# Optimization experiments

Hardware: AMD Instinct MI355X
Metric: run time of the kernel (lower is better)

Reference implementation:

```python
import jax, jax.numpy as jnp
import numpy as np

N_NODES = 50000
N_EDGES = 800000
N_GRAPHS = 32
IN_DIM = 3
HID = 128
EDGE_DIM = 3
OUT_DIM = 40
N_LAYERS = 3
EPS = 1e-5
SLOPE = 0.2  # GATv2 leaky_relu negative_slope


def setup_inputs() -> dict:
    key = jax.random.key(0)
    ks = jax.random.split(key, 24)
    s = lambda fan: 1.0 / np.sqrt(fan)
    inp = {
        "x": jax.random.normal(ks[0], (N_NODES, IN_DIM), jnp.float32),
        "edge_attr": jax.random.normal(ks[1], (N_EDGES, EDGE_DIM), jnp.float32),
        "edge_index": jax.random.randint(ks[2], (2, N_EDGES), 0, N_NODES),
        "batch": jnp.sort(jax.random.randint(ks[3], (N_NODES,), 0, N_GRAPHS)),
        # layer 0 (in_dim -> hid, separate lin_l / lin_r)
        "W0l": jax.random.normal(ks[4], (IN_DIM, HID), jnp.float32) * s(IN_DIM),
        "W0r": jax.random.normal(ks[5], (IN_DIM, HID), jnp.float32) * s(IN_DIM),
        "We0": jax.random.normal(ks[6], (EDGE_DIM, HID), jnp.float32) * s(EDGE_DIM),
        "a0": jax.random.normal(ks[7], (HID,), jnp.float32) * s(HID),
        "b0": jnp.zeros((HID,), jnp.float32),
        "bn0_g": jnp.ones((HID,), jnp.float32),
        "bn0_b": jnp.zeros((HID,), jnp.float32),
        # layers 1..n-1 (hid -> hid, share_weights=True -> single W per layer)
        "W": jax.random.normal(ks[8], (N_LAYERS - 1, HID, HID), jnp.float32) * s(HID),
        "We": jax.random.normal(ks[9], (N_LAYERS - 1, EDGE_DIM, HID), jnp.float32) * s(EDGE_DIM),
        "a": jax.random.normal(ks[10], (N_LAYERS - 1, HID), jnp.float32) * s(HID),
        "b": jnp.zeros((N_LAYERS - 1, HID), jnp.float32),
        "bn_g": jnp.ones((N_LAYERS - 1, HID), jnp.float32),
        "bn_b": jnp.zeros((N_LAYERS - 1, HID), jnp.float32),
        # FC classifier head (Linear-ReLU-Linear)
        "fc1_W": jax.random.normal(ks[11], (HID, HID), jnp.float32) * s(HID),
        "fc1_b": jnp.zeros((HID,), jnp.float32),
        "fc2_W": jax.random.normal(ks[12], (HID, OUT_DIM), jnp.float32) * s(HID),
        "fc2_b": jnp.zeros((OUT_DIM,), jnp.float32),
    }
    return inp


def _self_loop_attr(edge_attr, dst):
    # PyG add_self_loops(fill_value='mean'): per-node mean of incoming edge_attr
    cnt = jax.ops.segment_sum(jnp.ones((edge_attr.shape[0],), edge_attr.dtype), dst, num_segments=N_NODES)
    tot = jax.ops.segment_sum(edge_attr, dst, num_segments=N_NODES)
    return tot / jnp.maximum(cnt, 1.0)[:, None]


def _gatv2(x, src, dst, eattr, Wl, Wr, We, att, bias):
    xl = x @ Wl                                   # [N,H] source transform
    xr = x @ Wr                                   # [N,H] target transform
    e = eattr @ We                                # [E2,H]
    m = jax.nn.leaky_relu(xl[src] + xr[dst] + e, SLOPE)
    logit = m @ att                               # [E2]
    lmax = jax.ops.segment_max(logit, dst, num_segments=N_NODES)
    ex = jnp.exp(logit - lmax[dst])
    den = jax.ops.segment_sum(ex, dst, num_segments=N_NODES)
    alpha = ex / den[dst]
    out = jax.ops.segment_sum(alpha[:, None] * xl[src], dst, num_segments=N_NODES)
    return out + bias


def _bn(h, g, b):
    mu = h.mean(0)
    var = jnp.mean((h - mu) ** 2, 0)
    return g * (h - mu) * jax.lax.rsqrt(var + EPS) + b


def reference(x, edge_attr, edge_index, batch, W0l, W0r, We0, a0, b0, bn0_g, bn0_b,
              W, We, a, b, bn_g, bn_b, fc1_W, fc1_b, fc2_W, fc2_b):
    src, dst = edge_index[0], edge_index[1]
    loop = jnp.arange(N_NODES)
    loop_attr = _self_loop_attr(edge_attr, dst)
    src2 = jnp.concatenate([src, loop])
    dst2 = jnp.concatenate([dst, loop])
    eattr2 = jnp.concatenate([edge_attr, loop_attr], axis=0)

    h = _gatv2(x, src2, dst2, eattr2, W0l, W0r, We0, a0, b0)
    h = _bn(jax.nn.relu(h), bn0_g, bn0_b)
    for i in range(N_LAYERS - 1):  # share_weights=True: Wl == Wr == W[i]
        h = _gatv2(h, src2, dst2, eattr2, W[i], W[i], We[i], a[i], b[i])
        h = _bn(jax.nn.relu(h), bn_g[i], bn_b[i])

    pooled = jax.ops.segment_max(h, batch, num_segments=N_GRAPHS)  # [G,H]
    z = jax.nn.relu(pooled @ fc1_W + fc1_b)
    return z @ fc2_W + fc2_b  # [G, OUT_DIM]
```

## Files before the change

### kernel.cpp

```cpp
#include <hip/hip_runtime.h>

#define NN 50000
#define NE 800000
#define NG 32
#define HID 128
#define BNEPS 1e-5f
#define NETOT (NE + NN)

typedef float f32x2 __attribute__((ext_vector_type(2)));
typedef float f32x4 __attribute__((ext_vector_type(4)));
typedef short bf16x8 __attribute__((ext_vector_type(8)));

__device__ __forceinline__ unsigned fenc(float f) {
  unsigned u = __float_as_uint(f);
  return (u & 0x80000000u) ? ~u : (u | 0x80000000u);
}

__device__ __forceinline__ unsigned bfr(float f) {
  unsigned u = __float_as_uint(f);
  return (u + 0x7fffu + ((u >> 16) & 1u)) >> 16;
}
__device__ __forceinline__ unsigned pack2(float a, float b) {
  return bfr(a) | (bfr(b) << 16);
}
__device__ __forceinline__ float bf_lo(unsigned u) { return __uint_as_float(u << 16); }
__device__ __forceinline__ float bf_hi(unsigned u) { return __uint_as_float(u & 0xffff0000u); }

#define DPPADD(x, ctrl, rmask)                                                   \
  (x) += __int_as_float(__builtin_amdgcn_update_dpp(0, __float_as_int(x),        \
                                                    (ctrl), (rmask), 0xf, true))


__global__ __launch_bounds__(256) void k_hist(const int* __restrict__ ei,
                                              int* __restrict__ deg,
                                              int* __restrict__ pos) {
  int e = blockIdx.x * 256 + threadIdx.x;
  if (e >= NE) return;
  pos[e] = atomicAdd(&deg[ei[NE + e]], 1);
}

__global__ __launch_bounds__(1024) void k_scanA(const int* __restrict__ deg,
                                                int* __restrict__ rowp,
                                                int* __restrict__ bsum) {
  __shared__ int wsum[16];
  int t = threadIdx.x, lane = t & 63, w = t >> 6;
  int i = blockIdx.x * 1024 + t;
  int v = (i < NN) ? (deg[i] + 1) : 0;
  int s = v;
#pragma unroll
  for (int off = 1; off < 64; off <<= 1) {
    int y = __shfl_up(s, off, 64);
    if (lane >= off) s += y;
  }
  if (lane == 63) wsum[w] = s;
  __syncthreads();
  if (t < 16) {
    int xv = wsum[t];
#pragma unroll
    for (int off = 1; off < 16; off <<= 1) {
      int y = __shfl_up(xv, off, 64);
      if (t >= off) xv += y;
    }
    wsum[t] = xv;
  }
  __syncthreads();
  int wexcl = (w == 0) ? 0 : wsum[w - 1];
  int incl = wexcl + s;
  if (i < NN) rowp[i] = incl - v;
  if (t == 1023) bsum[blockIdx.x] = incl;
}

__global__ __launch_bounds__(64) void k_scanB(int* __restrict__ bsum,
                                              int* __restrict__ rowp,
                                              uint2* __restrict__ edat) {
  int t = threadIdx.x;
  int v = (t < 49) ? bsum[t] : 0;
  int s = v;
#pragma unroll
  for (int off = 1; off < 64; off <<= 1) {
    int y = __shfl_up(s, off, 64);
    if (t >= off) s += y;
  }
  bsum[t] = s - v;
  if (t == 48) rowp[NN] = s;
  for (int j = t; j < 256; j += 64) {
    uint2 z; z.x = 0u; z.y = 0u;
    edat[NETOT + j] = z;
  }
}

__global__ __launch_bounds__(1024) void k_scanC(int* __restrict__ rowp,
                                                const int* __restrict__ bsum) {
  int i = blockIdx.x * 1024 + threadIdx.x;
  if (i < NN) rowp[i] += bsum[blockIdx.x];
}

__global__ __launch_bounds__(256) void k_scatter(const int* __restrict__ ei,
    const float* __restrict__ eattr, const int* __restrict__ rowp,
    const int* __restrict__ pos, uint2* __restrict__ edat) {
  int e = blockIdx.x * 256 + threadIdx.x;
  if (e >= NE) return;
  int d = ei[NE + e];
  int p = rowp[d] + pos[e];
  uint2 v;
  v.x = (unsigned)ei[e] | (bfr(eattr[e * 3 + 0]) << 16);
  v.y = bfr(eattr[e * 3 + 1]) | (bfr(eattr[e * 3 + 2]) << 16);
  edat[p] = v;
}

__global__ __launch_bounds__(256) void k_selfmean(const int* __restrict__ rowp,
                                                  uint2* __restrict__ edat) {
  int n = blockIdx.x * 256 + threadIdx.x;
  if (n >= NN) return;
  int beg = rowp[n], endm1 = rowp[n + 1] - 1;
  float s0 = 0.f, s1 = 0.f, s2 = 0.f;
  for (int i = beg; i < endm1; ++i) {
    uint2 v = edat[i];
    s0 += bf_hi(v.x); s1 += bf_lo(v.y); s2 += bf_hi(v.y);
  }
  int cnt = endm1 - beg;
  float inv = cnt > 0 ? 1.f / (float)cnt : 0.f;
  uint2 o;
  o.x = (unsigned)n | (bfr(s0 * inv) << 16);
  o.y = bfr(s1 * inv) | (bfr(s2 * inv) << 16);
  edat[endm1] = o;
}


__global__ __launch_bounds__(256) void k_xform0(const float* __restrict__ x,
    const float* __restrict__ W0l, const float* __restrict__ W0r,
    unsigned* __restrict__ A, unsigned* __restrict__ B) {
  int t = blockIdx.x * 256 + threadIdx.x;
  int n = t >> 5;
  int c = (t & 31) * 4;
  if (n >= NN) return;
  float x0 = x[n * 3 + 0], x1 = x[n * 3 + 1], x2 = x[n * 3 + 2];
  float4 a0 = *(const float4*)&W0l[c];
  float4 a1 = *(const float4*)&W0l[HID + c];
  float4 a2 = *(const float4*)&W0l[2 * HID + c];
  float oax = x0 * a0.x + x1 * a1.x + x2 * a2.x;
  float oay = x0 * a0.y + x1 * a1.y + x2 * a2.y;
  float oaz = x0 * a0.z + x1 * a1.z + x2 * a2.z;
  float oaw = x0 * a0.w + x1 * a1.w + x2 * a2.w;
  uint2 pa;
  pa.x = pack2(oax, oay);
  pa.y = pack2(oaz, oaw);
  *(uint2*)&A[n * 64 + (c >> 1)] = pa;
  float4 b0 = *(const float4*)&W0r[c];
  float4 b1 = *(const float4*)&W0r[HID + c];
  float4 b2 = *(const float4*)&W0r[2 * HID + c];
  float obx = x0 * b0.x + x1 * b1.x + x2 * b2.x;
  float oby = x0 * b0.y + x1 * b1.y + x2 * b2.y;
  float obz = x0 * b0.z + x1 * b1.z + x2 * b2.z;
  float obw = x0 * b0.w + x1 * b1.w + x2 * b2.w;
  uint2 pb;
  pb.x = pack2(obx, oby);
  pb.y = pack2(obz, obw);
  *(uint2*)&B[n * 64 + (c >> 1)] = pb;
}


__global__ __launch_bounds__(256) void k_wprep(const float* __restrict__ W,
    const float* __restrict__ cs, const float* __restrict__ g,
    const float* __restrict__ b, unsigned* __restrict__ Wt,
    float* __restrict__ bias2) {
  __shared__ float scS[HID], shS[HID];
  int t = threadIdx.x;
  if (t < HID) {
    float mu = cs[t] * (1.f / NN);
    float var = fmaxf(cs[HID + t] * (1.f / NN) - mu * mu, 0.f);
    float sc = g[t] * rsqrtf(var + BNEPS);
    scS[t] = sc;
    shS[t] = b[t] - mu * sc;
  }
  __syncthreads();
  for (int i = t; i < HID * 64; i += 256) {
    int n = i >> 6, kp = (i & 63) * 2;
    Wt[i] = pack2(scS[kp] * W[kp * HID + n], scS[kp + 1] * W[(kp + 1) * HID + n]);
  }
  if (t < HID) {
    float acc = 0.f;
    for (int k = 0; k < HID; ++k) acc += shS[k] * W[k * HID + t];
    bias2[t] = acc;
  }
}


__global__ __launch_bounds__(256) void k_gemm(const unsigned* __restrict__ Hb,
    const unsigned* __restrict__ Wt, const float* __restrict__ bias2,
    unsigned* __restrict__ A) {
  __shared__ unsigned WsL[HID * 68];
  int t = threadIdx.x;
  for (int i = t; i < HID * 64; i += 256)
    WsL[(i >> 6) * 68 + (i & 63)] = Wt[i];
  __syncthreads();
  int l = t & 63;
  int w = t >> 6;
  int r0 = blockIdx.x * 64 + w * 16;
  int l15 = l & 15;
  int arow = min(r0 + l15, NN - 1);
  int kg = (l >> 4) * 4;
  float bl[8];
#pragma unroll
  for (int nt = 0; nt < 8; ++nt) bl[nt] = bias2[nt * 16 + l15];
  f32x4 acc[8] = {};
#pragma unroll
  for (int ks = 0; ks < 4; ++ks) {
    uint4 au = *(const uint4*)&Hb[arow * 64 + ks * 16 + kg];
    au.x &= ~(((au.x >> 15) & 0x10001u) * 0xFFFFu);
    au.y &= ~(((au.y >> 15) & 0x10001u) * 0xFFFFu);
    au.z &= ~(((au.z >> 15) & 0x10001u) * 0xFFFFu);
    au.w &= ~(((au.w >> 15) & 0x10001u) * 0xFFFFu);
    bf16x8 af = *(bf16x8*)&au;
#pragma unroll
    for (int nt = 0; nt < 8; ++nt) {
      uint4 bu = *(const uint4*)&WsL[(nt * 16 + l15) * 68 + ks * 16 + kg];
      bf16x8 bf = *(bf16x8*)&bu;
      acc[nt] = __builtin_amdgcn_mfma_f32_16x16x32_bf16(af, bf, acc[nt], 0, 0, 0);
    }
  }
#pragma unroll
  for (int nt = 0; nt < 8; ++nt) {
#pragma unroll
    for (int reg = 0; reg < 4; ++reg) {
      float v = acc[nt][reg] + bl[nt];
      float nb = __shfl_down(v, 1, 64);
      int rm = r0 + (l >> 4) * 4 + reg;
      if (((l & 1) == 0) && rm < NN)
        A[rm * 64 + nt * 8 + (l15 >> 1)] = pack2(v, nb);
    }
  }
}


__global__ __launch_bounds__(256) void k_edge(const unsigned* __restrict__ XL,
    const unsigned* __restrict__ XR, const uint2* __restrict__ edat,
    const int* __restrict__ rowp, const float* __restrict__ We,
    const float* __restrict__ att, const float* __restrict__ bias,
    unsigned* __restrict__ Hb) {
  __shared__ float WeS[3 * HID];
  int t = threadIdx.x;
  for (int i = t; i < 3 * HID; i += 256) WeS[i] = We[i];
  __syncthreads();
  int lane = t & 63;
  int l4 = lane & 15;
  int n = blockIdx.x * 16 + (t >> 6) * 4 + (lane >> 4);
  int c0 = l4 * 8;
  uint4 urx = *(const uint4*)&XR[n * 64 + l4 * 4];
  f32x2 xr0 = {bf_lo(urx.x), bf_hi(urx.x)};
  f32x2 xr1 = {bf_lo(urx.y), bf_hi(urx.y)};
  f32x2 xr2 = {bf_lo(urx.z), bf_hi(urx.z)};
  f32x2 xr3 = {bf_lo(urx.w), bf_hi(urx.w)};
  f32x2 at0 = *(const f32x2*)&att[c0];
  f32x2 at1 = *(const f32x2*)&att[c0 + 2];
  f32x2 at2 = *(const f32x2*)&att[c0 + 4];
  f32x2 at3 = *(const f32x2*)&att[c0 + 6];
  at0 *= 1.44269504f; at1 *= 1.44269504f; at2 *= 1.44269504f; at3 *= 1.44269504f;
  f32x2 w00 = *(const f32x2*)&WeS[c0],         w01 = *(const f32x2*)&WeS[c0 + 2];
  f32x2 w02 = *(const f32x2*)&WeS[c0 + 4],     w03 = *(const f32x2*)&WeS[c0 + 6];
  f32x2 w10 = *(const f32x2*)&WeS[HID + c0],   w11 = *(const f32x2*)&WeS[HID + c0 + 2];
  f32x2 w12 = *(const f32x2*)&WeS[HID + c0+4], w13 = *(const f32x2*)&WeS[HID + c0 + 6];
  f32x2 w20 = *(const f32x2*)&WeS[2*HID + c0],   w21 = *(const f32x2*)&WeS[2*HID + c0 + 2];
  f32x2 w22 = *(const f32x2*)&WeS[2*HID + c0+4], w23 = *(const f32x2*)&WeS[2*HID + c0 + 6];
  int beg = rowp[n], end = rowp[n + 1];
  int rem = end - beg;
  int tc = rem;
  tc = max(tc, __shfl_xor(tc, 16, 64));
  tc = max(tc, __shfl_xor(tc, 32, 64));
  int trips = (__builtin_amdgcn_readfirstlane(tc) + 3) & ~3;
  const unsigned* XLg = XL + l4 * 4;

  uint2 e0 = edat[beg], e1 = edat[beg + 1], e2 = edat[beg + 2], e3 = edat[beg + 3];
  uint4 x0 = *(const uint4*)&XLg[(e0.x & 0xffffu) * 64];
  uint4 x1 = *(const uint4*)&XLg[(e1.x & 0xffffu) * 64];
  uint4 x2, x3;
  f32x2 a0 = {0.f, 0.f}, a1 = {0.f, 0.f}, a2 = {0.f, 0.f}, a3 = {0.f, 0.f};
  float s = 0.f;

#define BODY(ED, XU, J)                                                           \
  {                                                                               \
    f32x2 xs0 = {bf_lo(XU.x), bf_hi(XU.x)};                                       \
    f32x2 xs1 = {bf_lo(XU.y), bf_hi(XU.y)};                                       \
    f32x2 xs2 = {bf_lo(XU.z), bf_hi(XU.z)};                                       \
    f32x2 xs3 = {bf_lo(XU.w), bf_hi(XU.w)};                                       \
    float ea0 = bf_hi(ED.x), ea1 = bf_lo(ED.y), ea2 = bf_hi(ED.y);                \
    f32x2 u0 = xs0 + xr0, u1 = xs1 + xr1, u2 = xs2 + xr2, u3 = xs3 + xr3;         \
    u0 = ea0 * w00 + u0; u1 = ea0 * w01 + u1; u2 = ea0 * w02 + u2; u3 = ea0 * w03 + u3; \
    u0 = ea1 * w10 + u0; u1 = ea1 * w11 + u1; u2 = ea1 * w12 + u2; u3 = ea1 * w13 + u3; \
    u0 = ea2 * w20 + u0; u1 = ea2 * w21 + u1; u2 = ea2 * w22 + u2; u3 = ea2 * w23 + u3; \
    f32x2 v0 = __builtin_elementwise_max(u0, 0.2f * u0);                          \
    f32x2 v1 = __builtin_elementwise_max(u1, 0.2f * u1);                          \
    f32x2 v2 = __builtin_elementwise_max(u2, 0.2f * u2);                          \
    f32x2 v3 = __builtin_elementwise_max(u3, 0.2f * u3);                          \
    f32x2 pl = v0 * at0;                                                          \
    pl = v1 * at1 + pl;                                                           \
    pl = v2 * at2 + pl;                                                           \
    pl = v3 * at3 + pl;                                                           \
    float part = pl.x + pl.y;                                                     \
    DPPADD(part, 0x121, 0xf);                                      \
    DPPADD(part, 0x122, 0xf);                                      \
    DPPADD(part, 0x124, 0xf);                                      \
    DPPADD(part, 0x128, 0xf);        \
    float p = __builtin_amdgcn_exp2f(part);                                       \
    p = (i + (J) < rem) ? p : 0.f;                                                \
    s += p;                                                                       \
    a0 = p * xs0 + a0; a1 = p * xs1 + a1;                                         \
    a2 = p * xs2 + a2; a3 = p * xs3 + a3;                                         \
  }

  for (int i = 0; i < trips; i += 4) {
    x2 = *(const uint4*)&XLg[(e2.x & 0xffffu) * 64];
    BODY(e0, x0, 0);
    e0 = edat[beg + i + 4];
    x3 = *(const uint4*)&XLg[(e3.x & 0xffffu) * 64];
    BODY(e1, x1, 1);
    e1 = edat[beg + i + 5];
    x0 = *(const uint4*)&XLg[(e0.x & 0xffffu) * 64];
    BODY(e2, x2, 2);
    e2 = edat[beg + i + 6];
    x1 = *(const uint4*)&XLg[(e1.x & 0xffffu) * 64];
    BODY(e3, x3, 3);
    e3 = edat[beg + i + 7];
  }
#undef BODY

  float inv = 1.f / s;
  f32x2 b0 = *(const f32x2*)&bias[c0];
  f32x2 b1 = *(const f32x2*)&bias[c0 + 2];
  f32x2 b2 = *(const f32x2*)&bias[c0 + 4];
  f32x2 b3 = *(const f32x2*)&bias[c0 + 6];
  f32x2 o0 = a0 * inv + b0;
  f32x2 o1 = a1 * inv + b1;
  f32x2 o2 = a2 * inv + b2;
  f32x2 o3 = a3 * inv + b3;
  uint4 o;
  o.x = pack2(o0.x, o0.y);
  o.y = pack2(o1.x, o1.y);
  o.z = pack2(o2.x, o2.y);
  o.w = pack2(o3.x, o3.y);
  *(uint4*)&Hb[n * 64 + l4 * 4] = o;
}


__global__ __launch_bounds__(256) void k_bnstats(const unsigned* __restrict__ Hb,
                                                 float* __restrict__ cs) {
  __shared__ float red[8][256];
  int t = threadIdx.x;
  int ui = (t & 31) * 2;
  int c0 = ui * 2;
  int grp = t >> 5;
  int chunk = (NN + gridDim.x - 1) / gridDim.x;
  int n0 = blockIdx.x * chunk, n1 = min(n0 + chunk, NN);
  float s10 = 0.f, s11 = 0.f, s12 = 0.f, s13 = 0.f;
  float s20 = 0.f, s21 = 0.f, s22 = 0.f, s23 = 0.f;
  for (int n = n0 + grp; n < n1; n += 8) {
    uint2 h = *(const uint2*)&Hb[n * 64 + ui];
    float v0 = fmaxf(bf_lo(h.x), 0.f), v1 = fmaxf(bf_hi(h.x), 0.f);
    float v2 = fmaxf(bf_lo(h.y), 0.f), v3 = fmaxf(bf_hi(h.y), 0.f);
    s10 += v0; s11 += v1; s12 += v2; s13 += v3;
    s20 += v0 * v0; s21 += v1 * v1; s22 += v2 * v2; s23 += v3 * v3;
  }
  red[grp][c0 + 0] = s10; red[grp][c0 + 1] = s11;
  red[grp][c0 + 2] = s12; red[grp][c0 + 3] = s13;
  red[grp][128 + c0 + 0] = s20; red[grp][128 + c0 + 1] = s21;
  red[grp][128 + c0 + 2] = s22; red[grp][128 + c0 + 3] = s23;
  __syncthreads();
  float sum = 0.f;
#pragma unroll
  for (int g2 = 0; g2 < 8; ++g2) sum += red[g2][t];
  atomicAdd(&cs[t], sum);
}


__global__ __launch_bounds__(256) void k_pool(const unsigned* __restrict__ Hb,
    const int* __restrict__ batch, const float* __restrict__ cs,
    const float* __restrict__ g, const float* __restrict__ b,
    unsigned* __restrict__ pooled) {
  int t = threadIdx.x;
  int ui = (t & 31) * 2;
  int c0 = ui * 2;
  int grp = t >> 5;
  float scv0, scv1, scv2, scv3, shv0, shv1, shv2, shv3;
  {
    float mu, var;
    mu = cs[c0 + 0] * (1.f / NN); var = fmaxf(cs[HID + c0 + 0] * (1.f / NN) - mu * mu, 0.f);
    scv0 = g[c0 + 0] * rsqrtf(var + BNEPS); shv0 = b[c0 + 0] - mu * scv0;
    mu = cs[c0 + 1] * (1.f / NN); var = fmaxf(cs[HID + c0 + 1] * (1.f / NN) - mu * mu, 0.f);
    scv1 = g[c0 + 1] * rsqrtf(var + BNEPS); shv1 = b[c0 + 1] - mu * scv1;
    mu = cs[c0 + 2] * (1.f / NN); var = fmaxf(cs[HID + c0 + 2] * (1.f / NN) - mu * mu, 0.f);
    scv2 = g[c0 + 2] * rsqrtf(var + BNEPS); shv2 = b[c0 + 2] - mu * scv2;
    mu = cs[c0 + 3] * (1.f / NN); var = fmaxf(cs[HID + c0 + 3] * (1.f / NN) - mu * mu, 0.f);
    scv3 = g[c0 + 3] * rsqrtf(var + BNEPS); shv3 = b[c0 + 3] - mu * scv3;
  }
  int chunk = (NN + gridDim.x - 1) / gridDim.x;
  int n0 = blockIdx.x * chunk, n1 = min(n0 + chunk, NN);
  int curg = -1;
  float m0 = -3.402823e38f, m1 = m0, m2 = m0, m3 = m0;
  for (int n = n0 + grp; n < n1; n += 8) {
    int gg = batch[n];
    if (gg != curg) {
      if (curg >= 0) {
        atomicMax(&pooled[curg * HID + c0 + 0], fenc(m0));
        atomicMax(&pooled[curg * HID + c0 + 1], fenc(m1));
        atomicMax(&pooled[curg * HID + c0 + 2], fenc(m2));
        atomicMax(&pooled[curg * HID + c0 + 3], fenc(m3));
      }
      curg = gg;
      m0 = m1 = m2 = m3 = -3.402823e38f;
    }
    uint2 h = *(const uint2*)&Hb[n * 64 + ui];
    m0 = fmaxf(m0, fmaxf(bf_lo(h.x), 0.f) * scv0 + shv0);
    m1 = fmaxf(m1, fmaxf(bf_hi(h.x), 0.f) * scv1 + shv1);
    m2 = fmaxf(m2, fmaxf(bf_lo(h.y), 0.f) * scv2 + shv2);
    m3 = fmaxf(m3, fmaxf(bf_hi(h.y), 0.f) * scv3 + shv3);
  }
  if (curg >= 0) {
    atomicMax(&pooled[curg * HID + c0 + 0], fenc(m0));
    atomicMax(&pooled[curg * HID + c0 + 1], fenc(m1));
    atomicMax(&pooled[curg * HID + c0 + 2], fenc(m2));
    atomicMax(&pooled[curg * HID + c0 + 3], fenc(m3));
  }
}


__global__ __launch_bounds__(128) void k_fc(const unsigned* __restrict__ pooled,
    const float* __restrict__ W1, const float* __restrict__ b1,
    const float* __restrict__ W2, const float* __restrict__ b2,
    float* __restrict__ out) {
  __shared__ float P[HID];
  __shared__ float Z[HID];
  int g = blockIdx.x, c = threadIdx.x;
  unsigned k = pooled[g * HID + c];
  P[c] = (k & 0x80000000u) ? __uint_as_float(k ^ 0x80000000u) : __uint_as_float(~k);
  __syncthreads();
  float acc = b1[c];
  for (int kk = 0; kk < HID; ++kk) acc += P[kk] * W1[kk * HID + c];
  Z[c] = fmaxf(acc, 0.f);
  __syncthreads();
  if (c < 40) {
    float a2 = b2[c];
    for (int kk = 0; kk < HID; ++kk) a2 += Z[kk] * W2[kk * 40 + c];
    out[g * 40 + c] = a2;
  }
}


extern "C" void kernel_launch(void* const* d_in, const int* in_sizes, int n_in,
                              void* d_out, int out_size, void* d_ws, size_t ws_size,
                              hipStream_t stream) {
  (void)in_sizes; (void)n_in; (void)out_size; (void)ws_size;
  const float* x     = (const float*)d_in[0];
  const float* eattr = (const float*)d_in[1];
  const int*   ei    = (const int*)d_in[2];
  const int*   batch = (const int*)d_in[3];
  const float* W0l   = (const float*)d_in[4];
  const float* W0r   = (const float*)d_in[5];
  const float* We0   = (const float*)d_in[6];
  const float* a0    = (const float*)d_in[7];
  const float* b0    = (const float*)d_in[8];
  const float* bn0g  = (const float*)d_in[9];
  const float* bn0b  = (const float*)d_in[10];
  const float* Wl    = (const float*)d_in[11];
  const float* Wel   = (const float*)d_in[12];
  const float* al    = (const float*)d_in[13];
  const float* bl    = (const float*)d_in[14];
  const float* bng   = (const float*)d_in[15];
  const float* bnb   = (const float*)d_in[16];
  const float* fc1W  = (const float*)d_in[17];
  const float* fc1b  = (const float*)d_in[18];
  const float* fc2W  = (const float*)d_in[19];
  const float* fc2b  = (const float*)d_in[20];
  float* out = (float*)d_out;

  char* ws = (char*)d_ws;
  unsigned* Hbf  = (unsigned*)(ws + 0);
  unsigned* Abf  = (unsigned*)(ws + 12800000);
  unsigned* X0bf = (unsigned*)(ws + 25600000);
  uint2*    edat = (uint2*)(ws + 38400000);
  int*      rowp = (int*)(ws + 45202048);
  int*      pos  = (int*)(ws + 45402112);
  char*     zb   = ws + 48602112;
  int*      deg  = (int*)(zb + 0);
  float*    cs   = (float*)(zb + 200000);
  unsigned* pooled = (unsigned*)(zb + 203072);
  int*      bsum = (int*)(zb + 219456);
  const size_t ZLEN = 219712;
  unsigned* wtb   = (unsigned*)(ws + 48821824);
  float*    bias2 = (float*)(ws + 48854592);

  hipMemsetAsync(zb, 0, ZLEN, stream);

  k_hist<<<(NE + 255) / 256, 256, 0, stream>>>(ei, deg, pos);
  k_scanA<<<49, 1024, 0, stream>>>(deg, rowp, bsum);
  k_scanB<<<1, 64, 0, stream>>>(bsum, rowp, edat);
  k_scanC<<<49, 1024, 0, stream>>>(rowp, bsum);
  k_scatter<<<(NE + 255) / 256, 256, 0, stream>>>(ei, eattr, rowp, pos, edat);
  k_selfmean<<<(NN + 255) / 256, 256, 0, stream>>>(rowp, edat);

  k_xform0<<<(NN * 32) / 256, 256, 0, stream>>>(x, W0l, W0r, Abf, X0bf);
  k_edge<<<(NN + 15) / 16, 256, 0, stream>>>(Abf, X0bf, edat, rowp, We0, a0, b0, Hbf);
  k_bnstats<<<512, 256, 0, stream>>>(Hbf, cs);

  k_wprep<<<1, 256, 0, stream>>>(Wl, cs, bn0g, bn0b, wtb, bias2);
  k_gemm<<<(NN + 63) / 64, 256, 0, stream>>>(Hbf, wtb, bias2, Abf);
  k_edge<<<(NN + 15) / 16, 256, 0, stream>>>(Abf, Abf, edat, rowp, Wel, al, bl, Hbf);
  k_bnstats<<<512, 256, 0, stream>>>(Hbf, cs + 256);

  k_wprep<<<1, 256, 0, stream>>>(Wl + 128 * 128, cs + 256, bng, bnb, wtb, bias2);
  k_gemm<<<(NN + 63) / 64, 256, 0, stream>>>(Hbf, wtb, bias2, Abf);
  k_edge<<<(NN + 15) / 16, 256, 0, stream>>>(Abf, Abf, edat, rowp, Wel + 384, al + 128, bl + 128, Hbf);
  k_bnstats<<<512, 256, 0, stream>>>(Hbf, cs + 512);

  k_pool<<<512, 256, 0, stream>>>(Hbf, batch, cs + 512, bng + 128, bnb + 128, pooled);
  k_fc<<<NG, 128, 0, stream>>>(pooled, fc1W, fc1b, fc2W, fc2b, out);
}
```

Before: 358.0 us.

## Sort destination nodes by in-degree to balance edge-kernel wavefronts

```diff
diff --git a/kernel.cpp b/kernel.cpp
--- a/kernel.cpp
+++ b/kernel.cpp
@@ -39,13 +39,60 @@
   pos[e] = atomicAdd(&deg[ei[NE + e]], 1);
 }
 
+
+__global__ __launch_bounds__(256) void k_dhist(const int* __restrict__ deg,
+                                               int* __restrict__ dhist) {
+  int n = blockIdx.x * 256 + threadIdx.x;
+  if (n >= NN) return;
+  atomicAdd(&dhist[min(deg[n], 1023)], 1);
+}
+
+__global__ __launch_bounds__(1024) void k_dscan(const int* __restrict__ dhist,
+                                                int* __restrict__ dbase) {
+  __shared__ int wsum[16];
+  int t = threadIdx.x, lane = t & 63, w = t >> 6;
+  int v = dhist[t];
+  int s = v;
+#pragma unroll
+  for (int off = 1; off < 64; off <<= 1) {
+    int y = __shfl_up(s, off, 64);
+    if (lane >= off) s += y;
+  }
+  if (lane == 63) wsum[w] = s;
+  __syncthreads();
+  if (t < 16) {
+    int xv = wsum[t];
+#pragma unroll
+    for (int off = 1; off < 16; off <<= 1) {
+      int y = __shfl_up(xv, off, 64);
+      if (t >= off) xv += y;
+    }
+    wsum[t] = xv;
+  }
+  __syncthreads();
+  int incl = s + ((w == 0) ? 0 : wsum[w - 1]);
+  dbase[t] = NN - incl;
+}
+
+__global__ __launch_bounds__(256) void k_dscatter(const int* __restrict__ deg,
+    const int* __restrict__ dbase, int* __restrict__ dfill,
+    int* __restrict__ ord, int* __restrict__ rank) {
+  int n = blockIdx.x * 256 + threadIdx.x;
+  if (n >= NN) return;
+  int d = min(deg[n], 1023);
+  int p = dbase[d] + atomicAdd(&dfill[d], 1);
+  ord[p] = n;
+  rank[n] = p;
+}
+
 __global__ __launch_bounds__(1024) void k_scanA(const int* __restrict__ deg,
+                                                const int* __restrict__ ord,
                                                 int* __restrict__ rowp,
                                                 int* __restrict__ bsum) {
   __shared__ int wsum[16];
   int t = threadIdx.x, lane = t & 63, w = t >> 6;
   int i = blockIdx.x * 1024 + t;
-  int v = (i < NN) ? (deg[i] + 1) : 0;
+  int v = (i < NN) ? (deg[ord[i]] + 1) : 0;
   int s = v;
 #pragma unroll
   for (int off = 1; off < 64; off <<= 1) {
@@ -97,11 +144,12 @@
 
 __global__ __launch_bounds__(256) void k_scatter(const int* __restrict__ ei,
     const float* __restrict__ eattr, const int* __restrict__ rowp,
-    const int* __restrict__ pos, uint2* __restrict__ edat) {
+    const int* __restrict__ pos, const int* __restrict__ rank,
+    uint2* __restrict__ edat) {
   int e = blockIdx.x * 256 + threadIdx.x;
   if (e >= NE) return;
   int d = ei[NE + e];
-  int p = rowp[d] + pos[e];
+  int p = rowp[rank[d]] + pos[e];
   uint2 v;
   v.x = (unsigned)ei[e] | (bfr(eattr[e * 3 + 0]) << 16);
   v.y = bfr(eattr[e * 3 + 1]) | (bfr(eattr[e * 3 + 2]) << 16);
@@ -109,6 +157,7 @@
 }
 
 __global__ __launch_bounds__(256) void k_selfmean(const int* __restrict__ rowp,
+                                                  const int* __restrict__ ord,
                                                   uint2* __restrict__ edat) {
   int n = blockIdx.x * 256 + threadIdx.x;
   if (n >= NN) return;
@@ -121,7 +170,7 @@
   int cnt = endm1 - beg;
   float inv = cnt > 0 ? 1.f / (float)cnt : 0.f;
   uint2 o;
-  o.x = (unsigned)n | (bfr(s0 * inv) << 16);
+  o.x = (unsigned)ord[n] | (bfr(s0 * inv) << 16);
   o.y = bfr(s1 * inv) | (bfr(s2 * inv) << 16);
   edat[endm1] = o;
 }
@@ -191,43 +240,47 @@
     unsigned* __restrict__ A) {
   __shared__ unsigned WsL[HID * 68];
   int t = threadIdx.x;
-  for (int i = t; i < HID * 64; i += 256)
-    WsL[(i >> 6) * 68 + (i & 63)] = Wt[i];
+  for (int i4 = t * 4; i4 < HID * 64; i4 += 1024) {
+    uint4 v = *(const uint4*)&Wt[i4];
+    *(uint4*)&WsL[(i4 >> 6) * 68 + (i4 & 63)] = v;
+  }
   __syncthreads();
   int l = t & 63;
   int w = t >> 6;
-  int r0 = blockIdx.x * 64 + w * 16;
   int l15 = l & 15;
-  int arow = min(r0 + l15, NN - 1);
   int kg = (l >> 4) * 4;
   float bl[8];
 #pragma unroll
   for (int nt = 0; nt < 8; ++nt) bl[nt] = bias2[nt * 16 + l15];
-  f32x4 acc[8] = {};
-#pragma unroll
-  for (int ks = 0; ks < 4; ++ks) {
-    uint4 au = *(const uint4*)&Hb[arow * 64 + ks * 16 + kg];
-    au.x &= ~(((au.x >> 15) & 0x10001u) * 0xFFFFu);
-    au.y &= ~(((au.y >> 15) & 0x10001u) * 0xFFFFu);
-    au.z &= ~(((au.z >> 15) & 0x10001u) * 0xFFFFu);
-    au.w &= ~(((au.w >> 15) & 0x10001u) * 0xFFFFu);
-    bf16x8 af = *(bf16x8*)&au;
+  for (int rb = blockIdx.x; rb * 64 < NN; rb += gridDim.x) {
+    int r0 = rb * 64 + w * 16;
+    int arow = min(r0 + l15, NN - 1);
+    f32x4 acc[8] = {};
+#pragma unroll
+    for (int ks = 0; ks < 4; ++ks) {
+      uint4 au = *(const uint4*)&Hb[arow * 64 + ks * 16 + kg];
+      au.x &= ~(((au.x >> 15) & 0x10001u) * 0xFFFFu);
+      au.y &= ~(((au.y >> 15) & 0x10001u) * 0xFFFFu);
+      au.z &= ~(((au.z >> 15) & 0x10001u) * 0xFFFFu);
+      au.w &= ~(((au.w >> 15) & 0x10001u) * 0xFFFFu);
+      bf16x8 af = *(bf16x8*)&au;
+#pragma unroll
+      for (int nt = 0; nt < 8; ++nt) {
+        uint4 bu = *(const uint4*)&WsL[(nt * 16 + l15) * 68 + ks * 16 + kg];
+        bf16x8 bf = *(bf16x8*)&bu;
+        acc[nt] = __builtin_amdgcn_mfma_f32_16x16x32_bf16(af, bf, acc[nt], 0, 0, 0);
+      }
+    }
 #pragma unroll
     for (int nt = 0; nt < 8; ++nt) {
-      uint4 bu = *(const uint4*)&WsL[(nt * 16 + l15) * 68 + ks * 16 + kg];
-      bf16x8 bf = *(bf16x8*)&bu;
-      acc[nt] = __builtin_amdgcn_mfma_f32_16x16x32_bf16(af, bf, acc[nt], 0, 0, 0);
-    }
-  }
-#pragma unroll
-  for (int nt = 0; nt < 8; ++nt) {
-#pragma unroll
-    for (int reg = 0; reg < 4; ++reg) {
-      float v = acc[nt][reg] + bl[nt];
-      float nb = __shfl_down(v, 1, 64);
-      int rm = r0 + (l >> 4) * 4 + reg;
-      if (((l & 1) == 0) && rm < NN)
-        A[rm * 64 + nt * 8 + (l15 >> 1)] = pack2(v, nb);
+#pragma unroll
+      for (int reg = 0; reg < 4; ++reg) {
+        float v = acc[nt][reg] + bl[nt];
+        float nb = __shfl_down(v, 1, 64);
+        int rm = r0 + (l >> 4) * 4 + reg;
+        if (((l & 1) == 0) && rm < NN)
+          A[rm * 64 + nt * 8 + (l15 >> 1)] = pack2(v, nb);
+      }
     }
   }
 }
@@ -235,9 +288,9 @@
 
 __global__ __launch_bounds__(256) void k_edge(const unsigned* __restrict__ XL,
     const unsigned* __restrict__ XR, const uint2* __restrict__ edat,
-    const int* __restrict__ rowp, const float* __restrict__ We,
-    const float* __restrict__ att, const float* __restrict__ bias,
-    unsigned* __restrict__ Hb) {
+    const int* __restrict__ rowp, const int* __restrict__ ord,
+    const float* __restrict__ We, const float* __restrict__ att,
+    const float* __restrict__ bias, unsigned* __restrict__ Hb) {
   __shared__ float WeS[3 * HID];
   int t = threadIdx.x;
   for (int i = t; i < 3 * HID; i += 256) WeS[i] = We[i];
@@ -245,8 +298,9 @@
   int lane = t & 63;
   int l4 = lane & 15;
   int n = blockIdx.x * 16 + (t >> 6) * 4 + (lane >> 4);
+  int orig = ord[n];
   int c0 = l4 * 8;
-  uint4 urx = *(const uint4*)&XR[n * 64 + l4 * 4];
+  uint4 urx = *(const uint4*)&XR[orig * 64 + l4 * 4];
   f32x2 xr0 = {bf_lo(urx.x), bf_hi(urx.x)};
   f32x2 xr1 = {bf_lo(urx.y), bf_hi(urx.y)};
   f32x2 xr2 = {bf_lo(urx.z), bf_hi(urx.z)};
@@ -338,7 +392,7 @@
   o.y = pack2(o1.x, o1.y);
   o.z = pack2(o2.x, o2.y);
   o.w = pack2(o3.x, o3.y);
-  *(uint4*)&Hb[n * 64 + l4 * 4] = o;
+  *(uint4*)&Hb[orig * 64 + l4 * 4] = o;
 }
 
 
@@ -479,36 +533,44 @@
   uint2*    edat = (uint2*)(ws + 38400000);
   int*      rowp = (int*)(ws + 45202048);
   int*      pos  = (int*)(ws + 45402112);
-  char*     zb   = ws + 48602112;
+  unsigned* wtb   = (unsigned*)(ws + 48602112);
+  float*    bias2 = (float*)(ws + 48634880);
+  int*      ord  = (int*)(ws + 48635392);
+  int*      rank = (int*)(ws + 48835392);
+  int*      dbase = (int*)(ws + 49035392);
+  char*     zb   = ws + 49039488;
   int*      deg  = (int*)(zb + 0);
   float*    cs   = (float*)(zb + 200000);
   unsigned* pooled = (unsigned*)(zb + 203072);
   int*      bsum = (int*)(zb + 219456);
-  const size_t ZLEN = 219712;
-  unsigned* wtb   = (unsigned*)(ws + 48821824);
-  float*    bias2 = (float*)(ws + 48854592);
+  int*      dhist = (int*)(zb + 219712);
+  int*      dfill = (int*)(zb + 223808);
+  const size_t ZLEN = 227904;
 
   hipMemsetAsync(zb, 0, ZLEN, stream);
 
   k_hist<<<(NE + 255) / 256, 256, 0, stream>>>(ei, deg, pos);
-  k_scanA<<<49, 1024, 0, stream>>>(deg, rowp, bsum);
+  k_dhist<<<(NN + 255) / 256, 256, 0, stream>>>(deg, dhist);
+  k_dscan<<<1, 1024, 0, stream>>>(dhist, dbase);
+  k_dscatter<<<(NN + 255) / 256, 256, 0, stream>>>(deg, dbase, dfill, ord, rank);
+  k_scanA<<<49, 1024, 0, stream>>>(deg, ord, rowp, bsum);
   k_scanB<<<1, 64, 0, stream>>>(bsum, rowp, edat);
   k_scanC<<<49, 1024, 0, stream>>>(rowp, bsum);
-  k_scatter<<<(NE + 255) / 256, 256, 0, stream>>>(ei, eattr, rowp, pos, edat);
-  k_selfmean<<<(NN + 255) / 256, 256, 0, stream>>>(rowp, edat);
+  k_scatter<<<(NE + 255) / 256, 256, 0, stream>>>(ei, eattr, rowp, pos, rank, edat);
+  k_selfmean<<<(NN + 255) / 256, 256, 0, stream>>>(rowp, ord, edat);
 
   k_xform0<<<(NN * 32) / 256, 256, 0, stream>>>(x, W0l, W0r, Abf, X0bf);
-  k_edge<<<(NN + 15) / 16, 256, 0, stream>>>(Abf, X0bf, edat, rowp, We0, a0, b0, Hbf);
+  k_edge<<<(NN + 15) / 16, 256, 0, stream>>>(Abf, X0bf, edat, rowp, ord, We0, a0, b0, Hbf);
   k_bnstats<<<512, 256, 0, stream>>>(Hbf, cs);
 
   k_wprep<<<1, 256, 0, stream>>>(Wl, cs, bn0g, bn0b, wtb, bias2);
-  k_gemm<<<(NN + 63) / 64, 256, 0, stream>>>(Hbf, wtb, bias2, Abf);
-  k_edge<<<(NN + 15) / 16, 256, 0, stream>>>(Abf, Abf, edat, rowp, Wel, al, bl, Hbf);
+  k_gemm<<<391, 256, 0, stream>>>(Hbf, wtb, bias2, Abf);
+  k_edge<<<(NN + 15) / 16, 256, 0, stream>>>(Abf, Abf, edat, rowp, ord, Wel, al, bl, Hbf);
   k_bnstats<<<512, 256, 0, stream>>>(Hbf, cs + 256);
 
   k_wprep<<<1, 256, 0, stream>>>(Wl + 128 * 128, cs + 256, bng, bnb, wtb, bias2);
-  k_gemm<<<(NN + 63) / 64, 256, 0, stream>>>(Hbf, wtb, bias2, Abf);
-  k_edge<<<(NN + 15) / 16, 256, 0, stream>>>(Abf, Abf, edat, rowp, Wel + 384, al + 128, bl + 128, Hbf);
+  k_gemm<<<391, 256, 0, stream>>>(Hbf, wtb, bias2, Abf);
+  k_edge<<<(NN + 15) / 16, 256, 0, stream>>>(Abf, Abf, edat, rowp, ord, Wel + 384, al + 128, bl + 128, Hbf);
   k_bnstats<<<512, 256, 0, stream>>>(Hbf, cs + 512);
 
   k_pool<<<512, 256, 0, stream>>>(Hbf, batch, cs + 512, bng + 128, bnb + 128, pooled);
```

Measured after the change: 553.3 us. 1.55x slower.
